# Kernel tuning notes

Measured on AMD Instinct MI355X. Metric: run time of the kernel, lower is better.

The kernel has to match this reference:

```python
import jax, jax.numpy as jnp
import numpy as np

B, L, C, V = 16, 600, 256, 256
OUT_SEQ = 6000
KSZ = 5
DILATIONS = (1, 2, 4)
N_BLOCKS = 10
COND = 256  # speaker(128) + noise(128)
TEMP = 10.0
EPS = 1e-5


def _ccbn(x, cond, gw, gb, bw, bb):
    # x: (B, C, L); conditional batch-norm: per-channel stats over (batch, length),
    # gamma/beta predicted from condition vector.
    mu = jnp.mean(x, axis=(0, 2), keepdims=True)
    var = jnp.var(x, axis=(0, 2), keepdims=True)
    xn = (x - mu) * jax.lax.rsqrt(var + EPS)
    gamma = 1.0 + cond @ gw + gb  # (B, C)
    beta = cond @ bw + bb         # (B, C)
    return xn * gamma[:, :, None] + beta[:, :, None]


def _conv1d(x, w, b, dil=1):
    # x: (B, C_in, L); w: (C_out, C_in, K)
    y = jax.lax.conv_general_dilated(
        x, w, window_strides=(1,), padding='SAME', rhs_dilation=(dil,),
        dimension_numbers=('NCH', 'OIH', 'NCH'))
    return y + b[None, :, None]


def setup_inputs() -> dict:
    key = jax.random.key(0)
    ks = jax.random.split(key, 20)
    s = 0.02
    inp = {
        'inputs': jax.random.randint(ks[0], (B, L), 0, V),
        'speaker_embeddings': jax.random.normal(ks[1], (B, 128), jnp.float32),
        'noise': jax.random.normal(ks[2], (B, 128), jnp.float32),
        'emb': jax.random.normal(ks[3], (V, C), jnp.float32) * s,
        # 10 blocks x 3 dilated convs
        'conv_w': jax.random.normal(ks[4], (N_BLOCKS, 3, C, C, KSZ), jnp.float32) * s,
        'conv_b': jnp.zeros((N_BLOCKS, 3, C), jnp.float32),
        # CCBN projections per conv (gamma/beta from condition)
        'g_w': jax.random.normal(ks[5], (N_BLOCKS, 3, COND, C), jnp.float32) * s,
        'g_b': jnp.zeros((N_BLOCKS, 3, C), jnp.float32),
        'b_w': jax.random.normal(ks[6], (N_BLOCKS, 3, COND, C), jnp.float32) * s,
        'b_b': jnp.zeros((N_BLOCKS, 3, C), jnp.float32),
        # TokenLength head: 2 CCBNs + conv1 (256->256,k1) + conv2 (256->1,k1)
        'tl_g_w': jax.random.normal(ks[7], (2, COND, C), jnp.float32) * s,
        'tl_g_b': jnp.zeros((2, C), jnp.float32),
        'tl_b_w': jax.random.normal(ks[8], (2, COND, C), jnp.float32) * s,
        'tl_b_b': jnp.zeros((2, C), jnp.float32),
        'tl_conv1_w': jax.random.normal(ks[9], (C, C, 1), jnp.float32) * s,
        'tl_conv1_b': jnp.zeros((C,), jnp.float32),
        'tl_conv2_w': jax.random.normal(ks[10], (1, C, 1), jnp.float32) * s,
        'tl_conv2_b': jnp.zeros((1,), jnp.float32),
    }
    return inp


def reference(inputs, speaker_embeddings, noise, emb, conv_w, conv_b,
              g_w, g_b, b_w, b_b, tl_g_w, tl_g_b, tl_b_w, tl_b_b,
              tl_conv1_w, tl_conv1_b, tl_conv2_w, tl_conv2_b):
    cond = jnp.concatenate([speaker_embeddings, noise], axis=-1)  # (B, COND)
    x = emb[inputs]                    # (B, L, C)
    x = jnp.transpose(x, (0, 2, 1))    # (B, C, L)

    # 10 unaligned blocks: residual stacks of CCBN -> ReLU -> dilated conv
    for blk in range(N_BLOCKS):
        y = x
        for j, d in enumerate(DILATIONS):
            y = jax.nn.relu(_ccbn(y, cond, g_w[blk, j], g_b[blk, j], b_w[blk, j], b_b[blk, j]))
            y = _conv1d(y, conv_w[blk, j], conv_b[blk, j], dil=d)
        x = x + y
    unaligned = x  # (B, C, L)

    # TokenLength head
    t = jax.nn.relu(_ccbn(unaligned, cond, tl_g_w[0], tl_g_b[0], tl_b_w[0], tl_b_b[0]))
    t = _conv1d(t, tl_conv1_w, tl_conv1_b)
    t = jax.nn.relu(_ccbn(t, cond, tl_g_w[1], tl_g_b[1], tl_b_w[1], tl_b_b[1]))
    t = _conv1d(t, tl_conv2_w, tl_conv2_b)  # (B, 1, L)
    token_lengths = jax.nn.relu(t[:, 0, :])  # (B, L)

    token_ends = jnp.cumsum(token_lengths, axis=-1)        # (B, L)
    token_centers = token_ends - token_lengths / 2.0        # (B, L)
    aligned_lengths = token_ends

    out_pos = jnp.arange(OUT_SEQ, dtype=jnp.float32)         # (OUT,)
    diff = token_centers[:, None, :] - out_pos[None, :, None]  # (B, OUT, L)
    logits = -(diff * diff) / TEMP
    weights = jax.nn.softmax(logits, axis=-1)                # (B, OUT, L)

    feats = jnp.transpose(unaligned, (0, 2, 1))              # (B, L, C)
    aligned_features = jnp.einsum('bol,blc->boc', weights, feats)  # (B, OUT, C)
    return aligned_features, aligned_lengths
```

## Files before the change

### kernel.cpp

```cpp
#include <hip/hip_runtime.h>
#include <math.h>
#include <stdint.h>

#define EPSv 1e-5f

typedef short short8 __attribute__((ext_vector_type(8)));
typedef float floatx4 __attribute__((ext_vector_type(4)));

__device__ __forceinline__ unsigned short f2bf(float x) {
  unsigned u = __float_as_uint(x);
  unsigned r = (u + 0x7fffu + ((u >> 16) & 1u)) >> 16;
  return (unsigned short)r;
}

__device__ __forceinline__ void gld_lds16(const void* g, void* l) {
  __builtin_amdgcn_global_load_lds(
      (const __attribute__((address_space(1))) unsigned*)(uintptr_t)g,
      (__attribute__((address_space(3))) unsigned*)(uintptr_t)l,
      16, 0, 0);
}

__global__ void k_zero(float* __restrict__ p) {
  p[blockIdx.x * 256 + threadIdx.x] = 0.f;
}

__global__ void k_gamma_beta(const float* __restrict__ spk, const float* __restrict__ noise,
                             const float* __restrict__ g_w, const float* __restrict__ g_b,
                             const float* __restrict__ b_w, const float* __restrict__ b_b,
                             const float* __restrict__ tl_g_w, const float* __restrict__ tl_g_b,
                             const float* __restrict__ tl_b_w, const float* __restrict__ tl_b_b,
                             float* __restrict__ gammas, float* __restrict__ betas) {
  __shared__ float condl[16*256];
  int t = threadIdx.x;
  for (int idx = t; idx < 4096; idx += 256) {
    int b = idx >> 8, k = idx & 255;
    condl[idx] = (k < 128) ? spk[b*128 + k] : noise[b*128 + k - 128];
  }
  __syncthreads();
  int i = blockIdx.x;
  const float *gw, *bw, *gbias, *bbias;
  if (i < 30) { gw = g_w + (size_t)i*65536; bw = b_w + (size_t)i*65536; gbias = g_b + i*256; bbias = b_b + i*256; }
  else { int j = i - 30; gw = tl_g_w + (size_t)j*65536; bw = tl_b_w + (size_t)j*65536; gbias = tl_g_b + j*256; bbias = tl_b_b + j*256; }
  int co = (t & 63) + blockIdx.y * 64;
  int slot = t >> 6;
  float g[4] = {0.f,0.f,0.f,0.f}, bt[4] = {0.f,0.f,0.f,0.f};
  for (int k = 0; k < 256; ++k) {
    float gwv = gw[k*256 + co];
    float bwv = bw[k*256 + co];
    #pragma unroll
    for (int bb = 0; bb < 4; ++bb) {
      float cv = condl[(slot*4 + bb)*256 + k];
      g[bb]  = fmaf(cv, gwv, g[bb]);
      bt[bb] = fmaf(cv, bwv, bt[bb]);
    }
  }
  #pragma unroll
  for (int bb = 0; bb < 4; ++bb) {
    int b = slot*4 + bb;
    gammas[i*4096 + b*256 + co] = 1.0f + g[bb] + gbias[co];
    betas [i*4096 + b*256 + co] = bt[bb] + bbias[co];
  }
}

template<int TAPS>
__device__ __forceinline__ void wprep_body(const float* __restrict__ src,
                                           unsigned short* __restrict__ dst,
                                           int cotile, int chunk, int t) {
  int cow = t >> 2, ci8 = (t & 3) * 8;
  const float* s0 = src + ((size_t)(cotile*64 + cow)*256 + chunk*32 + ci8)*TAPS;
  float v[8*TAPS];
  #pragma unroll
  for (int i = 0; i < 8*TAPS; ++i) v[i] = s0[i];
  unsigned short* dblk = dst + (size_t)cotile*(8*TAPS*4096) + (size_t)chunk*(TAPS*4096);
  #pragma unroll
  for (int tap = 0; tap < TAPS; ++tap) {
    unsigned hi2[4], lo2[4];
    #pragma unroll
    for (int jj = 0; jj < 4; ++jj) {
      float a = v[(jj*2+0)*TAPS + tap], b = v[(jj*2+1)*TAPS + tap];
      unsigned short ha = f2bf(a), hb = f2bf(b);
      unsigned short la = f2bf(a - __uint_as_float((unsigned)ha << 16));
      unsigned short lb = f2bf(b - __uint_as_float((unsigned)hb << 16));
      hi2[jj] = (unsigned)ha | ((unsigned)hb << 16);
      lo2[jj] = (unsigned)la | ((unsigned)lb << 16);
    }
    uint4 H; H.x = hi2[0]; H.y = hi2[1]; H.z = hi2[2]; H.w = hi2[3];
    uint4 L; L.x = lo2[0]; L.y = lo2[1]; L.z = lo2[2]; L.w = lo2[3];
    *(uint4*)(dblk + (size_t)(tap*2)*2048 + cow*32 + ci8) = H;
    *(uint4*)(dblk + (size_t)(tap*2+1)*2048 + cow*32 + ci8) = L;
  }
}

__global__ __launch_bounds__(256) void k_wprep(const float* __restrict__ conv_w,
                                               const float* __restrict__ tl_c1_w,
                                               unsigned short* __restrict__ wp) {
  int cc = blockIdx.x;
  int cotile = blockIdx.y >> 3, chunk = blockIdx.y & 7;
  if (cc == 30) wprep_body<1>(tl_c1_w, wp + (size_t)30*655360, cotile, chunk, threadIdx.x);
  else          wprep_body<5>(conv_w + (size_t)cc*327680, wp + (size_t)cc*655360, cotile, chunk, threadIdx.x);
}

__global__ void k_embed2(const int* __restrict__ inp, const float* __restrict__ emb,
                         float* __restrict__ x, float* __restrict__ stat0) {
  int bx = blockIdx.x;
  int c = threadIdx.x;
  int r0 = bx * 60;
  float s = 0.f, s2 = 0.f;
  for (int r = 0; r < 60; ++r) {
    int row = inp[r0 + r];
    float v = emb[(size_t)row*256 + c];
    x[(size_t)(r0 + r)*256 + c] = v;
    s += v; s2 = fmaf(v, v, s2);
  }
  atomicAdd(&stat0[c], s);
  atomicAdd(&stat0[256 + c], s2);
}

__global__ __launch_bounds__(256) void k_norm(const float* __restrict__ z,
                      const float* __restrict__ stat,
                      const float* __restrict__ gam, const float* __restrict__ bet,
                      unsigned short* __restrict__ zn) {
  __shared__ float s_sc[32];
  __shared__ float s_sh[32];
  int b = blockIdx.x, chunk = blockIdx.y, rg = blockIdx.z;
  int t = threadIdx.x;
  if (t < 32) {
    int c = chunk*32 + t;
    float s = stat[c], s2 = stat[256 + c];
    float mu = s * (1.0f/9600.0f);
    float var = s2 * (1.0f/9600.0f) - mu*mu;
    float rs = rsqrtf(var + EPSv);
    float scale = rs * gam[b*256 + c];
    s_sc[t] = scale;
    s_sh[t] = fmaf(-mu, scale, bet[b*256 + c]);
  }
  __syncthreads();
  int srow = t >> 3, fq = t & 7;
  float4 sc4 = *(const float4*)&s_sc[fq*4];
  float4 sh4 = *(const float4*)&s_sh[fq*4];
  unsigned short* zh = zn + ((size_t)b*8 + chunk)*54400 + fq*4;
  unsigned short* zl = zh + 27200;
  const float* zb = z + (size_t)b*600*256 + chunk*32 + fq*4;
  #pragma unroll
  for (int i = 0; i < 4; ++i) {
    int r = rg*128 + i*32 + srow;
    if (r < 680) {
      int l = r - 8;
      uint2 vh; vh.x = 0u; vh.y = 0u;
      uint2 vl; vl.x = 0u; vl.y = 0u;
      if (l >= 0 && l < 600) {
        float4 zv = *(const float4*)&zb[(size_t)l*256];
        float v0 = fmaxf(fmaf(zv.x, sc4.x, sh4.x), 0.f);
        float v1 = fmaxf(fmaf(zv.y, sc4.y, sh4.y), 0.f);
        float v2 = fmaxf(fmaf(zv.z, sc4.z, sh4.z), 0.f);
        float v3 = fmaxf(fmaf(zv.w, sc4.w, sh4.w), 0.f);
        unsigned short h0 = f2bf(v0), h1 = f2bf(v1), h2 = f2bf(v2), h3 = f2bf(v3);
        unsigned short e0 = f2bf(v0 - __uint_as_float((unsigned)h0 << 16));
        unsigned short e1 = f2bf(v1 - __uint_as_float((unsigned)h1 << 16));
        unsigned short e2 = f2bf(v2 - __uint_as_float((unsigned)h2 << 16));
        unsigned short e3 = f2bf(v3 - __uint_as_float((unsigned)h3 << 16));
        vh.x = (unsigned)h0 | ((unsigned)h1 << 16);
        vh.y = (unsigned)h2 | ((unsigned)h3 << 16);
        vl.x = (unsigned)e0 | ((unsigned)e1 << 16);
        vl.y = (unsigned)e2 | ((unsigned)e3 << 16);
      }
      *(uint2*)&zh[(size_t)r*40] = vh;
      *(uint2*)&zl[(size_t)r*40] = vl;
    }
  }
}

template<int TAPS>
__global__ __launch_bounds__(256) void k_convm(const unsigned short* __restrict__ zn,
                        float* __restrict__ out, float* __restrict__ stat_out,
                        const unsigned short* __restrict__ wpc,
                        const float* __restrict__ bias, int dil, int mode) {
  __shared__ __align__(16) unsigned short Zhi[3584];
  __shared__ __align__(16) unsigned short Zlo[3584];
  __shared__ float lsum[32];
  __shared__ float lsq[32];
  int t = threadIdx.x;
  int bx = blockIdx.x;
  int b  = bx / 10;
  int l0 = (bx % 10) * 64;
  int co0 = blockIdx.y * 32;
  int cobase = (blockIdx.y & 1) * 32;
  int PAD = ((TAPS - 1)/2) * dil;
  int w = t >> 6, lane = t & 63;
  int lsub = (w & 1) * 32, cosub = (w >> 1) * 16;
  int quad = lane >> 4, nlan = lane & 15;
  if (t < 32) { lsum[t] = 0.f; lsq[t] = 0.f; }

  floatx4 acc[2];
  acc[0] = (floatx4){0.f,0.f,0.f,0.f};
  acc[1] = (floatx4){0.f,0.f,0.f,0.f};

  const unsigned short* zbase = zn + (size_t)b*435200 + (size_t)(l0 - PAD + 8)*40 + (size_t)lane*8;
  int ar0 = (lsub + nlan) * 40 + quad * 8;
  int ar1 = ar0 + 640;

  for (int chunk = 0; chunk < 8; ++chunk) {
    __syncthreads();
    const unsigned short* pch = wpc + (size_t)((blockIdx.y >> 1)*8 + chunk) * (TAPS*4096);
    short8 bh[TAPS], bl[TAPS];
    int cw = (cobase + cosub + nlan)*32 + quad*8;
    #pragma unroll
    for (int tap = 0; tap < TAPS; ++tap) {
      bh[tap] = *(const short8*)(pch + (size_t)(tap*2)*2048 + cw);
      bl[tap] = *(const short8*)(pch + (size_t)(tap*2+1)*2048 + cw);
    }
    const unsigned short* srcp = zbase + (size_t)chunk*54400;
    for (int i = w; i < 14; i += 4) {
      int p = (i >= 7) ? 1 : 0;
      int k = i - p*7;
      const unsigned short* g = srcp + p*27200 + k*512;
      unsigned short* lp = (p ? Zlo : Zhi) + k*512;
      gld_lds16(g, lp);
    }
    __syncthreads();
    #pragma unroll
    for (int tap = 0; tap < TAPS; ++tap) {
      int sh = tap * dil * 40;
      short8 ah0 = *(const short8*)&Zhi[ar0 + sh];
      short8 ah1 = *(const short8*)&Zhi[ar1 + sh];
      short8 al0 = *(const short8*)&Zlo[ar0 + sh];
      short8 al1 = *(const short8*)&Zlo[ar1 + sh];
      acc[0] = __builtin_amdgcn_mfma_f32_16x16x32_bf16(ah0, bh[tap], acc[0], 0, 0, 0);
      acc[0] = __builtin_amdgcn_mfma_f32_16x16x32_bf16(ah0, bl[tap], acc[0], 0, 0, 0);
      acc[0] = __builtin_amdgcn_mfma_f32_16x16x32_bf16(al0, bh[tap], acc[0], 0, 0, 0);
      acc[1] = __builtin_amdgcn_mfma_f32_16x16x32_bf16(ah1, bh[tap], acc[1], 0, 0, 0);
      acc[1] = __builtin_amdgcn_mfma_f32_16x16x32_bf16(ah1, bl[tap], acc[1], 0, 0, 0);
      acc[1] = __builtin_amdgcn_mfma_f32_16x16x32_bf16(al1, bh[tap], acc[1], 0, 0, 0);
    }
  }

  float bsv = bias[co0 + cosub + nlan];
  float ssum = 0.f, ssq = 0.f;
  #pragma unroll
  for (int mt = 0; mt < 2; ++mt) {
    #pragma unroll
    for (int r = 0; r < 4; ++r) {
      int l = l0 + lsub + mt*16 + quad*4 + r;
      if (l < 600) {
        float v = acc[mt][r] + bsv;
        float* dst = &out[((size_t)(b*600 + l))*256 + co0 + cosub + nlan];
        if (mode) v += *dst;
        *dst = v;
        ssum += v;
        ssq = fmaf(v, v, ssq);
      }
    }
  }
  ssum += __shfl_xor(ssum, 16, 64);
  ssum += __shfl_xor(ssum, 32, 64);
  ssq  += __shfl_xor(ssq, 16, 64);
  ssq  += __shfl_xor(ssq, 32, 64);
  if (quad == 0) {
    atomicAdd(&lsum[cosub + nlan], ssum);
    atomicAdd(&lsq [cosub + nlan], ssq);
  }
  __syncthreads();
  if (t < 32) {
    atomicAdd(&stat_out[co0 + t], lsum[t]);
    atomicAdd(&stat_out[256 + co0 + t], lsq[t]);
  }
}

__global__ void k_tl2(const float* __restrict__ z, const float* __restrict__ stat,
                      const float* __restrict__ gam, const float* __restrict__ bet,
                      const float* __restrict__ w2, const float* __restrict__ b2,
                      float* __restrict__ tl) {
  int t = threadIdx.x;
  int row = blockIdx.x * 4 + (t >> 6);
  int lane = t & 63;
  int b = row / 600;
  float4 s1 = *(const float4*)&stat[lane*4];
  float4 s2 = *(const float4*)&stat[256 + lane*4];
  float4 gm = *(const float4*)&gam[b*256 + lane*4];
  float4 bt = *(const float4*)&bet[b*256 + lane*4];
  float sc[4], sh[4];
  {
    float sv[4] = {s1.x, s1.y, s1.z, s1.w};
    float qv[4] = {s2.x, s2.y, s2.z, s2.w};
    float gv[4] = {gm.x, gm.y, gm.z, gm.w};
    float bv[4] = {bt.x, bt.y, bt.z, bt.w};
    #pragma unroll
    for (int i = 0; i < 4; ++i) {
      float mu = sv[i] * (1.0f/9600.0f);
      float var = qv[i] * (1.0f/9600.0f) - mu*mu;
      float rs = rsqrtf(var + EPSv);
      sc[i] = rs * gv[i];
      sh[i] = fmaf(-mu, sc[i], bv[i]);
    }
  }
  float4 zr = *(const float4*)&z[(size_t)row*256 + lane*4];
  float4 wr = *(const float4*)&w2[lane*4];
  float z0 = fmaxf(fmaf(zr.x, sc[0], sh[0]), 0.f);
  float z1 = fmaxf(fmaf(zr.y, sc[1], sh[1]), 0.f);
  float z2 = fmaxf(fmaf(zr.z, sc[2], sh[2]), 0.f);
  float z3 = fmaxf(fmaf(zr.w, sc[3], sh[3]), 0.f);
  float s = z0*wr.x + z1*wr.y + z2*wr.z + z3*wr.w;
  for (int m = 32; m >= 1; m >>= 1) s += __shfl_xor(s, m, 64);
  if (lane == 0) tl[row] = fmaxf(s + b2[0], 0.f);
}

__global__ void k_cumsum(const float* __restrict__ tl, float* __restrict__ centers,
                         float* __restrict__ out_len) {
  int b = blockIdx.x; int lane = threadIdx.x;
  float carry = 0.f;
  for (int ch = 0; ch < 10; ++ch) {
    int l = ch*64 + lane;
    float v = (l < 600) ? tl[b*600 + l] : 0.f;
    float s = v;
    #pragma unroll
    for (int off = 1; off < 64; off <<= 1) {
      float n = __shfl_up(s, off, 64);
      if (lane >= off) s += n;
    }
    float ends = carry + s;
    if (l < 600) {
      centers[b*600 + l] = ends - 0.5f*v;
      out_len[b*600 + l] = ends;
    }
    carry = __shfl(ends, 63, 64);
  }
}

__global__ void k_tobf16(const float* __restrict__ x, unsigned short* __restrict__ fbT) {
  __shared__ unsigned short T[64*66];
  int b = blockIdx.x, lt = blockIdx.y, ct = blockIdx.z;
  int t = threadIdx.x;
  int i4 = t >> 6;
  int j = t & 63;
  #pragma unroll
  for (int r = 0; r < 16; ++r) {
    int li = i4*16 + r;
    int l = lt*64 + li;
    float v = (l < 600) ? x[((size_t)(b*600 + l))*256 + ct*64 + j] : 0.f;
    T[j*66 + li] = f2bf(v);
  }
  __syncthreads();
  int row = t >> 2, seg = (t & 3) * 16;
  unsigned vv[8];
  #pragma unroll
  for (int k = 0; k < 8; ++k)
    vv[k] = *(const unsigned*)&T[row*66 + seg + k*2];
  size_t dsth = ((size_t)(b*256 + ct*64 + row))*640 + lt*64 + seg;
  unsigned* du = (unsigned*)fbT;
  uint4 a; a.x = vv[0]; a.y = vv[1]; a.z = vv[2]; a.w = vv[3];
  uint4 c4; c4.x = vv[4]; c4.y = vv[5]; c4.z = vv[6]; c4.w = vv[7];
  *(uint4*)(du + dsth/2) = a;
  *(uint4*)(du + dsth/2 + 4) = c4;
}

__global__ __launch_bounds__(256) void k_align2(const unsigned short* __restrict__ fbT,
                        const float* __restrict__ centers, float* __restrict__ outp) {
  __shared__ float cen[600];
  __shared__ float mrow[64];
  __shared__ float isum[64];
  __shared__ unsigned short Wt[64*72];
  __shared__ unsigned short Ft[256*72];
  int b = blockIdx.x;
  int o0 = blockIdx.y * 64;
  int t = threadIdx.x;
  int wv = t >> 6, lane = t & 63;
  for (int i = t; i < 600; i += 256) cen[i] = centers[b*600 + i];
  __syncthreads();
  for (int rr = 0; rr < 16; ++rr) {
    int oi = wv*16 + rr;
    float opos = (float)(o0 + oi);
    float mx = -3.0e38f;
    for (int l = lane; l < 600; l += 64) {
      float d = cen[l] - opos;
      mx = fmaxf(mx, -d*d*0.1f);
    }
    #pragma unroll
    for (int mm = 32; mm >= 1; mm >>= 1) mx = fmaxf(mx, __shfl_xor(mx, mm, 64));
    if (lane == 0) mrow[oi] = mx;
  }
  __syncthreads();
  floatx4 acc[4][4];
  #pragma unroll
  for (int i = 0; i < 4; ++i)
    #pragma unroll
    for (int j = 0; j < 4; ++j)
      acc[i][j] = (floatx4){0.f, 0.f, 0.f, 0.f};
  int quad = lane >> 4;
  int nlan = lane & 15;
  int oi_w = t >> 2;
  int sbase = t & 3;
  float mo = mrow[oi_w];
  float opos_w = (float)(o0 + oi_w);
  float psum = 0.f;
  const unsigned short* srcb = fbT + ((size_t)b*256)*640;

  for (int ch = 0; ch < 10; ++ch) {
    int lc0 = ch * 64;
    __syncthreads();
    #pragma unroll
    for (int sidx = 0; sidx < 2; ++sidx) {
      int seg = sbase + sidx*4;
      unsigned pk[4];
      #pragma unroll
      for (int jj = 0; jj < 8; jj += 2) {
        int li = lc0 + seg*8 + jj;
        float e0 = 0.f, e1 = 0.f;
        if (li < 600)     { float d = cen[li] - opos_w;     e0 = __expf(-d*d*0.1f - mo); }
        if (li + 1 < 600) { float d = cen[li + 1] - opos_w; e1 = __expf(-d*d*0.1f - mo); }
        psum += e0 + e1;
        pk[jj>>1] = (unsigned)f2bf(e0) | ((unsigned)f2bf(e1) << 16);
      }
      uint4 v; v.x = pk[0]; v.y = pk[1]; v.z = pk[2]; v.w = pk[3];
      *(uint4*)&Wt[oi_w*72 + seg*8] = v;
    }
    #pragma unroll
    for (int it = 0; it < 8; ++it) {
      int idx = t + it*256;
      int c = idx >> 3, part = idx & 7;
      uint4 v = *(const uint4*)(srcb + (size_t)c*640 + lc0 + part*8);
      *(uint4*)&Ft[c*72 + part*8] = v;
    }
    __syncthreads();
    #pragma unroll
    for (int ks = 0; ks < 2; ++ks) {
      int ko = ks*32 + quad*8;
      short8 af[4], bfr[4];
      #pragma unroll
      for (int mt = 0; mt < 4; ++mt)
        af[mt] = *(const short8*)&Wt[(mt*16 + nlan)*72 + ko];
      #pragma unroll
      for (int nt = 0; nt < 4; ++nt)
        bfr[nt] = *(const short8*)&Ft[(wv*64 + nt*16 + nlan)*72 + ko];
      #pragma unroll
      for (int mt = 0; mt < 4; ++mt)
        #pragma unroll
        for (int nt = 0; nt < 4; ++nt)
          acc[mt][nt] = __builtin_amdgcn_mfma_f32_16x16x32_bf16(af[mt], bfr[nt], acc[mt][nt], 0, 0, 0);
    }
  }
  psum += __shfl_xor(psum, 1, 64);
  psum += __shfl_xor(psum, 2, 64);
  if ((t & 3) == 0) isum[oi_w] = 1.0f / psum;
  __syncthreads();
  #pragma unroll
  for (int mt = 0; mt < 4; ++mt) {
    #pragma unroll
    for (int r = 0; r < 4; ++r) {
      int oi = mt*16 + quad*4 + r;
      int o = o0 + oi;
      if (o < 6000) {
        float sc = isum[oi];
        #pragma unroll
        for (int nt = 0; nt < 4; ++nt) {
          int c = wv*64 + nt*16 + nlan;
          outp[((size_t)b*6000 + o)*256 + c] = acc[mt][nt][r] * sc;
        }
      }
    }
  }
}

extern "C" void kernel_launch(void* const* d_in, const int* in_sizes, int n_in,
                              void* d_out, int out_size, void* d_ws, size_t ws_size,
                              hipStream_t stream) {
  const int*   inputs = (const int*)  d_in[0];
  const float* spk    = (const float*)d_in[1];
  const float* noise  = (const float*)d_in[2];
  const float* emb    = (const float*)d_in[3];
  const float* conv_w = (const float*)d_in[4];
  const float* conv_b = (const float*)d_in[5];
  const float* g_w    = (const float*)d_in[6];
  const float* g_b    = (const float*)d_in[7];
  const float* b_w    = (const float*)d_in[8];
  const float* b_b    = (const float*)d_in[9];
  const float* tl_g_w = (const float*)d_in[10];
  const float* tl_g_b = (const float*)d_in[11];
  const float* tl_b_w = (const float*)d_in[12];
  const float* tl_b_b = (const float*)d_in[13];
  const float* tl_c1_w = (const float*)d_in[14];
  const float* tl_c1_b = (const float*)d_in[15];
  const float* tl_c2_w = (const float*)d_in[16];
  const float* tl_c2_b = (const float*)d_in[17];
  float* out = (float*)d_out;

  float* ws = (float*)d_ws;
  float* x       = ws;
  float* A       = x + 2457600;
  float* Bf      = A + 2457600;
  float* gammas  = Bf + 2457600;
  float* betas   = gammas + 131072;
  float* statacc = betas + 131072;
  float* tl      = statacc + 16384;
  float* cen     = tl + 9600;
  unsigned short* wp = (unsigned short*)(cen + 9600);
  unsigned short* Zn = wp + (size_t)31*655360;
  unsigned short* fbT = (unsigned short*)Bf;

  k_zero<<<dim3(64), dim3(256), 0, stream>>>(statacc);
  k_wprep<<<dim3(31, 32), dim3(256), 0, stream>>>(conv_w, tl_c1_w, wp);
  k_gamma_beta<<<dim3(32, 4), dim3(256), 0, stream>>>(spk, noise, g_w, g_b, b_w, b_b,
      tl_g_w, tl_g_b, tl_b_w, tl_b_b, gammas, betas);
  k_embed2<<<dim3(160), dim3(256), 0, stream>>>(inputs, emb, x, statacc);

  const int dils[3] = {1, 2, 4};
  for (int blk = 0; blk < 10; ++blk) {
    const float* srcs[3] = {x, A, Bf};
    float*       dsts[3] = {A, Bf, x};
    for (int j = 0; j < 3; ++j) {
      int idx = blk*3 + j;
      int mode = (j == 2) ? 1 : 0;
      k_norm<<<dim3(16, 8, 6), dim3(256), 0, stream>>>(srcs[j],
          statacc + idx*512, gammas + idx*4096, betas + idx*4096, Zn);
      k_convm<5><<<dim3(160, 8), dim3(256), 0, stream>>>(Zn, dsts[j],
          statacc + (idx+1)*512,
          wp + (size_t)idx*655360, conv_b + idx*256, dils[j], mode);
    }
  }
  k_norm<<<dim3(16, 8, 6), dim3(256), 0, stream>>>(x,
      statacc + 30*512, gammas + 30*4096, betas + 30*4096, Zn);
  k_convm<1><<<dim3(160, 8), dim3(256), 0, stream>>>(Zn, A,
      statacc + 31*512,
      wp + (size_t)30*655360, tl_c1_b, 1, 0);
  k_tl2<<<dim3(2400), dim3(256), 0, stream>>>(A, statacc + 31*512,
      gammas + 31*4096, betas + 31*4096, tl_c2_w, tl_c2_b, tl);
  k_cumsum<<<dim3(16), dim3(64), 0, stream>>>(tl, cen, out + 24576000);
  k_tobf16<<<dim3(16, 10, 4), dim3(256), 0, stream>>>(x, fbT);
  k_align2<<<dim3(16, 94), dim3(256), 0, stream>>>(fbT, cen, out);
}
```

Before: 1.692 ms.

## Double-buffer LDS activation tiles in conv kernel to overlap loads with MFMA

Doubles the LDS buffers for the hi/lo activation tiles in the conv MFMA kernel. The next channel chunk is prefetched with global_load_lds while the current chunk is computed, and the two barriers per chunk become one. This is meant to hide global-to-LDS load latency behind the matrix ops, at the cost of twice the LDS footprint, which may reduce occupancy. The single barrier at the end of each iteration has to cover both the async load completion and the reuse of the buffer.

```diff
diff --git a/kernel.cpp b/kernel.cpp
--- a/kernel.cpp
+++ b/kernel.cpp
@@ -175,8 +175,8 @@
                         float* __restrict__ out, float* __restrict__ stat_out,
                         const unsigned short* __restrict__ wpc,
                         const float* __restrict__ bias, int dil, int mode) {
-  __shared__ __align__(16) unsigned short Zhi[3584];
-  __shared__ __align__(16) unsigned short Zlo[3584];
+  __shared__ __align__(16) unsigned short Zhi[2][3584];
+  __shared__ __align__(16) unsigned short Zlo[2][3584];
   __shared__ float lsum[32];
   __shared__ float lsq[32];
   int t = threadIdx.x;
@@ -199,8 +199,21 @@
   int ar0 = (lsub + nlan) * 40 + quad * 8;
   int ar1 = ar0 + 640;
 
+  #define STAGE(ch, bf) do {                                            \
+    const unsigned short* srcp = zbase + (size_t)(ch)*54400;            \
+    for (int i = w; i < 14; i += 4) {                                   \
+      int p = (i >= 7) ? 1 : 0;                                         \
+      int k = i - p*7;                                                  \
+      gld_lds16(srcp + p*27200 + k*512, (p ? Zlo[bf] : Zhi[bf]) + k*512); \
+    }                                                                   \
+  } while (0)
+
+  STAGE(0, 0);
+  __syncthreads();
+
   for (int chunk = 0; chunk < 8; ++chunk) {
-    __syncthreads();
+    int cb = chunk & 1;
+    if (chunk < 7) STAGE(chunk + 1, cb ^ 1);
     const unsigned short* pch = wpc + (size_t)((blockIdx.y >> 1)*8 + chunk) * (TAPS*4096);
     short8 bh[TAPS], bl[TAPS];
     int cw = (cobase + cosub + nlan)*32 + quad*8;
@@ -209,22 +222,13 @@
       bh[tap] = *(const short8*)(pch + (size_t)(tap*2)*2048 + cw);
       bl[tap] = *(const short8*)(pch + (size_t)(tap*2+1)*2048 + cw);
     }
-    const unsigned short* srcp = zbase + (size_t)chunk*54400;
-    for (int i = w; i < 14; i += 4) {
-      int p = (i >= 7) ? 1 : 0;
-      int k = i - p*7;
-      const unsigned short* g = srcp + p*27200 + k*512;
-      unsigned short* lp = (p ? Zlo : Zhi) + k*512;
-      gld_lds16(g, lp);
-    }
-    __syncthreads();
     #pragma unroll
     for (int tap = 0; tap < TAPS; ++tap) {
       int sh = tap * dil * 40;
-      short8 ah0 = *(const short8*)&Zhi[ar0 + sh];
-      short8 ah1 = *(const short8*)&Zhi[ar1 + sh];
-      short8 al0 = *(const short8*)&Zlo[ar0 + sh];
-      short8 al1 = *(const short8*)&Zlo[ar1 + sh];
+      short8 ah0 = *(const short8*)&Zhi[cb][ar0 + sh];
+      short8 ah1 = *(const short8*)&Zhi[cb][ar1 + sh];
+      short8 al0 = *(const short8*)&Zlo[cb][ar0 + sh];
+      short8 al1 = *(const short8*)&Zlo[cb][ar1 + sh];
       acc[0] = __builtin_amdgcn_mfma_f32_16x16x32_bf16(ah0, bh[tap], acc[0], 0, 0, 0);
       acc[0] = __builtin_amdgcn_mfma_f32_16x16x32_bf16(ah0, bl[tap], acc[0], 0, 0, 0);
       acc[0] = __builtin_amdgcn_mfma_f32_16x16x32_bf16(al0, bh[tap], acc[0], 0, 0, 0);
@@ -232,7 +236,9 @@
       acc[1] = __builtin_amdgcn_mfma_f32_16x16x32_bf16(ah1, bl[tap], acc[1], 0, 0, 0);
       acc[1] = __builtin_amdgcn_mfma_f32_16x16x32_bf16(al1, bh[tap], acc[1], 0, 0, 0);
     }
-  }
+    __syncthreads();
+  }
+  #undef STAGE
 
   float bsv = bias[co0 + cosub + nlan];
   float ssum = 0.f, ssq = 0.f;
```

New measurement: 1.670 ms. Within noise of the previous version (-1.3%).
